# Kernel optimization log

Hardware: AMD Instinct MI355X
Metric: run time of the kernel (lower is better)

Reference implementation:

```python
import jax, jax.numpy as jnp
import numpy as np

N_NODES = 50000
N_EDGES = 1600000
IN_DIM = 128
OUT_DIM = 128


def setup_inputs() -> dict:
    key = jax.random.key(0)
    k_h, k_e, k_wm, k_wu, k_bu = jax.random.split(key, 5)
    h = jax.random.normal(k_h, (N_NODES, IN_DIM), dtype=jnp.float32)
    edge_index = jax.random.randint(k_e, (2, N_EDGES), 0, N_NODES, dtype=jnp.int64)
    # nn.Linear weights: W_msg [out, in] no bias; W_upd [out, in+out] with bias
    s1 = 1.0 / np.sqrt(IN_DIM)
    s2 = 1.0 / np.sqrt(IN_DIM + OUT_DIM)
    W_msg = jax.random.uniform(k_wm, (OUT_DIM, IN_DIM), jnp.float32, -s1, s1)
    W_upd = jax.random.uniform(k_wu, (OUT_DIM, IN_DIM + OUT_DIM), jnp.float32, -s2, s2)
    b_upd = jax.random.uniform(k_bu, (OUT_DIM,), jnp.float32, -s2, s2)
    return {"h": h, "edge_index": edge_index, "W_msg": W_msg, "W_upd": W_upd, "b_upd": b_upd}


def reference(h, edge_index, W_msg, W_upd, b_upd):
    src, dst = edge_index[0], edge_index[1]
    # gather -> linear: messages [E, out_dim]
    messages = jnp.einsum("ei,oi->eo", h[src], W_msg)
    # scatter-add aggregation into [N, out_dim]
    agg = jax.ops.segment_sum(messages, dst, num_segments=h.shape[0])
    # concat -> linear -> relu
    hu = jnp.concatenate([h, agg], axis=1)
    return jax.nn.relu(jnp.einsum("ni,oi->no", hu, W_upd) + b_upd)
```

## Files before the change

### kernel.cpp

```cpp
#include <hip/hip_runtime.h>
#include <hip/hip_bf16.h>

#define NN   50000
#define NE   1600000
#define D    128
#define NBUK 391
#define CAP  5120
#define EPB  4096
#define ASTR 136

typedef __attribute__((ext_vector_type(8))) short short8;
typedef __attribute__((ext_vector_type(4))) float f32x4;

__device__ __forceinline__ unsigned short f2b(float x) {
  unsigned u = __float_as_uint(x);
  u += 0x7fffu + ((u >> 16) & 1u);
  return (unsigned short)(u >> 16);
}
__device__ __forceinline__ float b2f(unsigned short v) {
  return __uint_as_float(((unsigned)v) << 16);
}

__global__ __launch_bounds__(256) void init_k(const float* __restrict__ h,
                                              unsigned short* __restrict__ hb,
                                              int* __restrict__ gcur,
                                              const float* __restrict__ Wm,
                                              const float* __restrict__ Wu,
                                              unsigned short* __restrict__ W1b,
                                              unsigned short* __restrict__ Wcb,
                                              const int* __restrict__ ei,
                                              int* __restrict__ flg) {
  __shared__ int nz;
  const int blk = blockIdx.x;
  if (blk < 6250) {
    int i = blk * 256 + threadIdx.x;
    float4 x = ((const float4*)h)[i];
    ushort4 o;
    o.x = f2b(x.x); o.y = f2b(x.y); o.z = f2b(x.z); o.w = f2b(x.w);
    ((ushort4*)hb)[i] = o;
    if (i < NBUK) gcur[i] = 0;
  } else if (blk < 6314) {
    int tid = (blk - 6250) * 256 + threadIdx.x;
    int o = tid >> 7, j = tid & 127;
    W1b[tid] = f2b(Wu[o * 256 + j]);
    float acc = 0.f;
#pragma unroll 4
    for (int k = 0; k < 128; ++k)
      acc += Wu[o * 256 + 128 + k] * Wm[k * 128 + j];
    Wcb[tid] = f2b(acc);
  } else {
    if (threadIdx.x == 0) nz = 0;
    __syncthreads();
    int idx = 1 + 2 * ((int)threadIdx.x * (NE / 256));
    if (ei[idx] != 0) atomicOr(&nz, 1);
    __syncthreads();
    if (threadIdx.x == 0) *flg = (nz == 0) ? 1 : 0;
  }
}

__global__ __launch_bounds__(512) void bfill_k(const int* __restrict__ ei,
                                               const int* __restrict__ flag,
                                               int* __restrict__ gcur,
                                               unsigned* __restrict__ ebuf) {
  __shared__ int cnt[NBUK];
  __shared__ int off[NBUK];
  const int tid = threadIdx.x;
  if (tid < NBUK) cnt[tid] = 0;
  __syncthreads();
  const int f = *flag;
  const int e0 = blockIdx.x * EPB + tid * 8;
  unsigned pk[8]; int bk[8]; int lr[8];
  if (e0 + 8 <= NE) {
    int sv[8], dv[8];
    if (f) {
      const int4* ps = (const int4*)(ei + 2 * (size_t)e0);
      const int4* pd = (const int4*)(ei + 2 * (size_t)NE + 2 * (size_t)e0);
      int4 a = ps[0], b = ps[1], c = ps[2], d = ps[3];
      sv[0]=a.x; sv[1]=a.z; sv[2]=b.x; sv[3]=b.z; sv[4]=c.x; sv[5]=c.z; sv[6]=d.x; sv[7]=d.z;
      a = pd[0]; b = pd[1]; c = pd[2]; d = pd[3];
      dv[0]=a.x; dv[1]=a.z; dv[2]=b.x; dv[3]=b.z; dv[4]=c.x; dv[5]=c.z; dv[6]=d.x; dv[7]=d.z;
    } else {
      const int4* ps = (const int4*)(ei + e0);
      const int4* pd = (const int4*)(ei + (size_t)NE + e0);
      int4 a = ps[0], b = ps[1];
      sv[0]=a.x; sv[1]=a.y; sv[2]=a.z; sv[3]=a.w; sv[4]=b.x; sv[5]=b.y; sv[6]=b.z; sv[7]=b.w;
      a = pd[0]; b = pd[1];
      dv[0]=a.x; dv[1]=a.y; dv[2]=a.z; dv[3]=a.w; dv[4]=b.x; dv[5]=b.y; dv[6]=b.z; dv[7]=b.w;
    }
#pragma unroll
    for (int j = 0; j < 8; ++j) {
      bk[j] = dv[j] >> 7;
      pk[j] = (unsigned)sv[j] | ((unsigned)(dv[j] & 127) << 16);
      lr[j] = atomicAdd(&cnt[bk[j]], 1);
    }
  } else {
    for (int j = 0; j < 8; ++j) {
      int e = e0 + j;
      bk[j] = -1;
      if (e < NE) {
        int src = f ? ei[2 * (size_t)e] : ei[e];
        int dst = f ? ei[2 * ((size_t)NE + e)] : ei[NE + e];
        bk[j] = dst >> 7;
        pk[j] = (unsigned)src | ((unsigned)(dst & 127) << 16);
        lr[j] = atomicAdd(&cnt[bk[j]], 1);
      }
    }
  }
  __syncthreads();
  if (tid < NBUK)
    off[tid] = cnt[tid] ? atomicAdd(&gcur[tid], cnt[tid]) : 0;
  __syncthreads();
#pragma unroll
  for (int j = 0; j < 8; ++j) {
    if (bk[j] >= 0) {
      int idx = off[bk[j]] + lr[j];
      if (idx < CAP) ebuf[(size_t)bk[j] * CAP + idx] = pk[j];
    }
  }
}

__global__ __launch_bounds__(1024, 8) void sortagg_k(const unsigned* __restrict__ ebuf,
                                                     const int* __restrict__ gcur,
                                                     const unsigned short* __restrict__ hb,
                                                     const unsigned short* __restrict__ W1b,
                                                     const unsigned short* __restrict__ Wcb,
                                                     const float* __restrict__ bias,
                                                     float* __restrict__ out) {
  __shared__ unsigned short srt[CAP];
  __shared__ __align__(16) unsigned short aggL[128 * ASTR];
  __shared__ int cnt[128];
  __shared__ int ofs[129];
  __shared__ int cur[128];
  __shared__ int wsum[2];
  const int b = blockIdx.x, tid = threadIdx.x;
  const int lane = tid & 63, wv = tid >> 6;
  if (tid < 128) cnt[tid] = 0;
  __syncthreads();
  const int count = min(gcur[b], CAP);
  const unsigned* eb = ebuf + (size_t)b * CAP;
  for (int e = tid; e < count; e += 1024)
    atomicAdd(&cnt[eb[e] >> 16], 1);
  __syncthreads();
  int v = 0, s = 0;
  if (tid < 128) {
    v = cnt[tid]; s = v;
#pragma unroll
    for (int d = 1; d < 64; d <<= 1) {
      int t = __shfl_up(s, d, 64);
      if (lane >= d) s += t;
    }
    if (lane == 63) wsum[wv] = s;
  }
  __syncthreads();
  if (tid < 128) {
    int excl = (wv ? wsum[0] : 0) + s - v;
    ofs[tid] = excl;
    cur[tid] = excl;
  }
  if (tid == 0) ofs[128] = count;
  __syncthreads();
  for (int e = tid; e < count; e += 1024) {
    unsigned p = eb[e];
    int slot = atomicAdd(&cur[p >> 16], 1);
    srt[slot] = (unsigned short)(p & 0xffffu);
  }
  __syncthreads();

  const int l2 = lane * 2;
  const unsigned short* hbl = hb + l2;
#pragma unroll 1
  for (int k = 0; k < 8; ++k) {
    const int n = wv * 8 + k;
    const int beg = ofs[n], end = ofs[n + 1];
    float ax0 = 0.f, ay0 = 0.f, ax1 = 0.f, ay1 = 0.f;
    int e = beg;
    for (; e + 16 <= end; e += 16) {
      unsigned vv[16];
#pragma unroll
      for (int j = 0; j < 16; ++j)
        vv[j] = *(const unsigned*)(hbl + (size_t)srt[e + j] * D);
#pragma unroll
      for (int j = 0; j < 16; j += 2) {
        ax0 += b2f((unsigned short)(vv[j] & 0xffffu));
        ay0 += b2f((unsigned short)(vv[j] >> 16));
        ax1 += b2f((unsigned short)(vv[j + 1] & 0xffffu));
        ay1 += b2f((unsigned short)(vv[j + 1] >> 16));
      }
    }
    for (; e + 4 <= end; e += 4) {
      unsigned vv[4];
#pragma unroll
      for (int j = 0; j < 4; ++j)
        vv[j] = *(const unsigned*)(hbl + (size_t)srt[e + j] * D);
#pragma unroll
      for (int j = 0; j < 4; j += 2) {
        ax0 += b2f((unsigned short)(vv[j] & 0xffffu));
        ay0 += b2f((unsigned short)(vv[j] >> 16));
        ax1 += b2f((unsigned short)(vv[j + 1] & 0xffffu));
        ay1 += b2f((unsigned short)(vv[j + 1] >> 16));
      }
    }
    for (; e < end; ++e) {
      unsigned vv = *(const unsigned*)(hbl + (size_t)srt[e] * D);
      ax0 += b2f((unsigned short)(vv & 0xffffu));
      ay0 += b2f((unsigned short)(vv >> 16));
    }
    unsigned o = (unsigned)f2b(ax0 + ax1) | ((unsigned)f2b(ay0 + ay1) << 16);
    ((unsigned*)aggL)[n * (ASTR / 2) + lane] = o;
  }
  __syncthreads();

  const int r = lane & 15, g = lane >> 4;
  const int tile = wv >> 1;
  const int t0 = (wv & 1) * 4;
  const int rowL = tile * 16 + r;
  const int nodeA = min(b * 128 + rowL, NN - 1);

  f32x4 acc[4];
#pragma unroll
  for (int t = 0; t < 4; ++t) acc[t] = (f32x4){0.f, 0.f, 0.f, 0.f};

#pragma unroll
  for (int c = 0; c < 8; ++c) {
    const int k0 = (c & 3) * 32 + g * 8;
    short8 a;
    if (c < 4) {
      a = *(const short8*)(hb + (size_t)nodeA * D + k0);
    } else {
      a = *(const short8*)(aggL + rowL * ASTR + k0);
    }
    const unsigned short* W = (c < 4) ? W1b : Wcb;
#pragma unroll
    for (int tt = 0; tt < 4; ++tt) {
      short8 bfr = *(const short8*)(W + (size_t)((t0 + tt) * 16 + r) * D + k0);
      acc[tt] = __builtin_amdgcn_mfma_f32_16x16x32_bf16(a, bfr, acc[tt], 0, 0, 0);
    }
  }

#pragma unroll
  for (int tt = 0; tt < 4; ++tt) {
    const int col = (t0 + tt) * 16 + r;
    const float bv = bias[col];
#pragma unroll
    for (int j = 0; j < 4; ++j) {
      const int orow = b * 128 + tile * 16 + g * 4 + j;
      if (orow < NN) {
        float vv = acc[tt][j] + bv;
        out[(size_t)orow * D + col] = vv > 0.f ? vv : 0.f;
      }
    }
  }
}

extern "C" void kernel_launch(void* const* d_in, const int* in_sizes, int n_in,
                              void* d_out, int out_size, void* d_ws, size_t ws_size,
                              hipStream_t stream) {
  const float* h  = (const float*)d_in[0];
  const int*   ei = (const int*)d_in[1];
  const float* Wm = (const float*)d_in[2];
  const float* Wu = (const float*)d_in[3];
  const float* bu = (const float*)d_in[4];
  float* out = (float*)d_out;

  char* ws = (char*)d_ws;
  unsigned short* hb   = (unsigned short*)(ws);
  unsigned*       ebuf = (unsigned*)(ws + 12800000);
  int*            gcur = (int*)(ws + 20807680);
  unsigned short* W1b  = (unsigned short*)(ws + 20809728);
  unsigned short* Wcb  = (unsigned short*)(ws + 20842496);
  int*            flg  = (int*)(ws + 20875264);

  init_k<<<6315, 256, 0, stream>>>(h, hb, gcur, Wm, Wu, W1b, Wcb, ei, flg);
  bfill_k<<<(NE + EPB - 1) / EPB, 512, 0, stream>>>(ei, flg, gcur, ebuf);
  sortagg_k<<<NBUK, 1024, 0, stream>>>(ebuf, gcur, hb, W1b, Wcb, bu, out);
}
```

Before: 117.4 us.

## Fuse prep and bucket-fill kernels, widen gather loads, halve aggregation block size

Merges the bf16 conversion, weight folding, index-format detection and edge bucketing into one launch, replacing the gcur reset with a memset and computing the int64 flag inside each bucketing block. The aggregation kernel now runs 512 threads. Each wave handles 16 nodes, with 16-byte gathers spread over four edges per lane group and a shuffle reduction at the end. Each wave then computes a full 16x128 MFMA output tile. This aims to cut launch overhead and raise memory-level parallelism in the gather, at the cost of more registers per thread and redundant flag reads in every bucketing block.

```diff
diff --git a/kernel.cpp b/kernel.cpp
--- a/kernel.cpp
+++ b/kernel.cpp
@@ -8,6 +8,8 @@
 #define CAP  5120
 #define EPB  4096
 #define ASTR 136
+#define PREP_BLKS 3125
+#define WPREP_BLKS 32
 
 typedef __attribute__((ext_vector_type(8))) short short8;
 typedef __attribute__((ext_vector_type(4))) float f32x4;
@@ -17,58 +19,60 @@
   u += 0x7fffu + ((u >> 16) & 1u);
   return (unsigned short)(u >> 16);
 }
-__device__ __forceinline__ float b2f(unsigned short v) {
-  return __uint_as_float(((unsigned)v) << 16);
-}
-
-__global__ __launch_bounds__(256) void init_k(const float* __restrict__ h,
-                                              unsigned short* __restrict__ hb,
-                                              int* __restrict__ gcur,
-                                              const float* __restrict__ Wm,
-                                              const float* __restrict__ Wu,
-                                              unsigned short* __restrict__ W1b,
-                                              unsigned short* __restrict__ Wcb,
-                                              const int* __restrict__ ei,
-                                              int* __restrict__ flg) {
-  __shared__ int nz;
-  const int blk = blockIdx.x;
-  if (blk < 6250) {
-    int i = blk * 256 + threadIdx.x;
-    float4 x = ((const float4*)h)[i];
-    ushort4 o;
-    o.x = f2b(x.x); o.y = f2b(x.y); o.z = f2b(x.z); o.w = f2b(x.w);
-    ((ushort4*)hb)[i] = o;
-    if (i < NBUK) gcur[i] = 0;
-  } else if (blk < 6314) {
-    int tid = (blk - 6250) * 256 + threadIdx.x;
-    int o = tid >> 7, j = tid & 127;
-    W1b[tid] = f2b(Wu[o * 256 + j]);
-    float acc = 0.f;
-#pragma unroll 4
-    for (int k = 0; k < 128; ++k)
-      acc += Wu[o * 256 + 128 + k] * Wm[k * 128 + j];
-    Wcb[tid] = f2b(acc);
-  } else {
-    if (threadIdx.x == 0) nz = 0;
-    __syncthreads();
-    int idx = 1 + 2 * ((int)threadIdx.x * (NE / 256));
-    if (ei[idx] != 0) atomicOr(&nz, 1);
-    __syncthreads();
-    if (threadIdx.x == 0) *flg = (nz == 0) ? 1 : 0;
-  }
-}
-
-__global__ __launch_bounds__(512) void bfill_k(const int* __restrict__ ei,
-                                               const int* __restrict__ flag,
+__device__ __forceinline__ float b2f(unsigned v) {
+  return __uint_as_float(v << 16);
+}
+__device__ __forceinline__ float b2fh(unsigned v) {
+  return __uint_as_float(v & 0xffff0000u);
+}
+
+__global__ __launch_bounds__(512) void fused_k(const float* __restrict__ h,
+                                               unsigned short* __restrict__ hb,
                                                int* __restrict__ gcur,
+                                               const float* __restrict__ Wm,
+                                               const float* __restrict__ Wu,
+                                               unsigned short* __restrict__ W1b,
+                                               unsigned short* __restrict__ Wcb,
+                                               const int* __restrict__ ei,
                                                unsigned* __restrict__ ebuf) {
   __shared__ int cnt[NBUK];
   __shared__ int off[NBUK];
-  const int tid = threadIdx.x;
+  __shared__ int nz;
+  const int blk = blockIdx.x, tid = threadIdx.x;
+
+  if (blk >= NBUK) {
+    if (blk < NBUK + PREP_BLKS) {
+      int i = (blk - NBUK) * 512 + tid;
+      float4 x = ((const float4*)h)[i];
+      ushort4 o;
+      o.x = f2b(x.x); o.y = f2b(x.y); o.z = f2b(x.z); o.w = f2b(x.w);
+      ((ushort4*)hb)[i] = o;
+    } else {
+      int t2 = (blk - NBUK - PREP_BLKS) * 512 + tid;
+      if (t2 < 16384) {
+        int o = t2 >> 7, j = t2 & 127;
+        W1b[t2] = f2b(Wu[o * 256 + j]);
+        float acc = 0.f;
+#pragma unroll 4
+        for (int k = 0; k < 128; ++k)
+          acc += Wu[o * 256 + 128 + k] * Wm[k * 128 + j];
+        Wcb[t2] = f2b(acc);
+      }
+    }
+    return;
+  }
+
+  if (tid == 0) nz = 0;
   if (tid < NBUK) cnt[tid] = 0;
   __syncthreads();
-  const int f = *flag;
-  const int e0 = blockIdx.x * EPB + tid * 8;
+  if (tid < 256) {
+    int idx = 1 + 2 * (tid * (NE / 256));
+    if (ei[idx] != 0) atomicOr(&nz, 1);
+  }
+  __syncthreads();
+  const int f = (nz == 0);
+
+  const int e0 = blk * EPB + tid * 8;
   unsigned pk[8]; int bk[8]; int lr[8];
   if (e0 + 8 <= NE) {
     int sv[8], dv[8];
@@ -119,13 +123,13 @@
   }
 }
 
-__global__ __launch_bounds__(1024, 8) void sortagg_k(const unsigned* __restrict__ ebuf,
-                                                     const int* __restrict__ gcur,
-                                                     const unsigned short* __restrict__ hb,
-                                                     const unsigned short* __restrict__ W1b,
-                                                     const unsigned short* __restrict__ Wcb,
-                                                     const float* __restrict__ bias,
-                                                     float* __restrict__ out) {
+__global__ __launch_bounds__(512, 6) void sortagg_k(const unsigned* __restrict__ ebuf,
+                                                    const int* __restrict__ gcur,
+                                                    const unsigned short* __restrict__ hb,
+                                                    const unsigned short* __restrict__ W1b,
+                                                    const unsigned short* __restrict__ Wcb,
+                                                    const float* __restrict__ bias,
+                                                    float* __restrict__ out) {
   __shared__ unsigned short srt[CAP];
   __shared__ __align__(16) unsigned short aggL[128 * ASTR];
   __shared__ int cnt[128];
@@ -138,7 +142,7 @@
   __syncthreads();
   const int count = min(gcur[b], CAP);
   const unsigned* eb = ebuf + (size_t)b * CAP;
-  for (int e = tid; e < count; e += 1024)
+  for (int e = tid; e < count; e += 512)
     atomicAdd(&cnt[eb[e] >> 16], 1);
   __syncthreads();
   int v = 0, s = 0;
@@ -159,66 +163,71 @@
   }
   if (tid == 0) ofs[128] = count;
   __syncthreads();
-  for (int e = tid; e < count; e += 1024) {
+  for (int e = tid; e < count; e += 512) {
     unsigned p = eb[e];
     int slot = atomicAdd(&cur[p >> 16], 1);
     srt[slot] = (unsigned short)(p & 0xffffu);
   }
   __syncthreads();
 
-  const int l2 = lane * 2;
-  const unsigned short* hbl = hb + l2;
+  const int q = lane >> 4;
+  const int r = lane & 15;
+  const unsigned short* hbl = hb + r * 8;
 #pragma unroll 1
-  for (int k = 0; k < 8; ++k) {
-    const int n = wv * 8 + k;
+  for (int k = 0; k < 16; ++k) {
+    const int n = wv * 16 + k;
     const int beg = ofs[n], end = ofs[n + 1];
-    float ax0 = 0.f, ay0 = 0.f, ax1 = 0.f, ay1 = 0.f;
+    float a0=0.f,a1=0.f,a2=0.f,a3=0.f,a4=0.f,a5=0.f,a6=0.f,a7=0.f;
     int e = beg;
-    for (; e + 16 <= end; e += 16) {
-      unsigned vv[16];
-#pragma unroll
-      for (int j = 0; j < 16; ++j)
-        vv[j] = *(const unsigned*)(hbl + (size_t)srt[e + j] * D);
-#pragma unroll
-      for (int j = 0; j < 16; j += 2) {
-        ax0 += b2f((unsigned short)(vv[j] & 0xffffu));
-        ay0 += b2f((unsigned short)(vv[j] >> 16));
-        ax1 += b2f((unsigned short)(vv[j + 1] & 0xffffu));
-        ay1 += b2f((unsigned short)(vv[j + 1] >> 16));
-      }
-    }
-    for (; e + 4 <= end; e += 4) {
-      unsigned vv[4];
-#pragma unroll
-      for (int j = 0; j < 4; ++j)
-        vv[j] = *(const unsigned*)(hbl + (size_t)srt[e + j] * D);
-#pragma unroll
-      for (int j = 0; j < 4; j += 2) {
-        ax0 += b2f((unsigned short)(vv[j] & 0xffffu));
-        ay0 += b2f((unsigned short)(vv[j] >> 16));
-        ax1 += b2f((unsigned short)(vv[j + 1] & 0xffffu));
-        ay1 += b2f((unsigned short)(vv[j + 1] >> 16));
-      }
-    }
-    for (; e < end; ++e) {
-      unsigned vv = *(const unsigned*)(hbl + (size_t)srt[e] * D);
-      ax0 += b2f((unsigned short)(vv & 0xffffu));
-      ay0 += b2f((unsigned short)(vv >> 16));
-    }
-    unsigned o = (unsigned)f2b(ax0 + ax1) | ((unsigned)f2b(ay0 + ay1) << 16);
-    ((unsigned*)aggL)[n * (ASTR / 2) + lane] = o;
-  }
-  __syncthreads();
-
-  const int r = lane & 15, g = lane >> 4;
-  const int tile = wv >> 1;
-  const int t0 = (wv & 1) * 4;
-  const int rowL = tile * 16 + r;
+    for (; e + 32 <= end; e += 32) {
+      uint4 vv[8];
+#pragma unroll
+      for (int j = 0; j < 8; ++j)
+        vv[j] = *(const uint4*)(hbl + (size_t)srt[e + 4 * j + q] * D);
+#pragma unroll
+      for (int j = 0; j < 8; ++j) {
+        a0 += b2f(vv[j].x & 0xffffu); a1 += b2fh(vv[j].x);
+        a2 += b2f(vv[j].y & 0xffffu); a3 += b2fh(vv[j].y);
+        a4 += b2f(vv[j].z & 0xffffu); a5 += b2fh(vv[j].z);
+        a6 += b2f(vv[j].w & 0xffffu); a7 += b2fh(vv[j].w);
+      }
+    }
+    for (; e < end; e += 4) {
+      int edge = e + q;
+      int ce = min(edge, end - 1);
+      uint4 vv = *(const uint4*)(hbl + (size_t)srt[ce] * D);
+      if (edge >= end) { vv.x = 0u; vv.y = 0u; vv.z = 0u; vv.w = 0u; }
+      a0 += b2f(vv.x & 0xffffu); a1 += b2fh(vv.x);
+      a2 += b2f(vv.y & 0xffffu); a3 += b2fh(vv.y);
+      a4 += b2f(vv.z & 0xffffu); a5 += b2fh(vv.z);
+      a6 += b2f(vv.w & 0xffffu); a7 += b2fh(vv.w);
+    }
+    a0 += __shfl_xor(a0, 16, 64); a0 += __shfl_xor(a0, 32, 64);
+    a1 += __shfl_xor(a1, 16, 64); a1 += __shfl_xor(a1, 32, 64);
+    a2 += __shfl_xor(a2, 16, 64); a2 += __shfl_xor(a2, 32, 64);
+    a3 += __shfl_xor(a3, 16, 64); a3 += __shfl_xor(a3, 32, 64);
+    a4 += __shfl_xor(a4, 16, 64); a4 += __shfl_xor(a4, 32, 64);
+    a5 += __shfl_xor(a5, 16, 64); a5 += __shfl_xor(a5, 32, 64);
+    a6 += __shfl_xor(a6, 16, 64); a6 += __shfl_xor(a6, 32, 64);
+    a7 += __shfl_xor(a7, 16, 64); a7 += __shfl_xor(a7, 32, 64);
+    if (lane < 16) {
+      uint4 o;
+      o.x = (unsigned)f2b(a0) | ((unsigned)f2b(a1) << 16);
+      o.y = (unsigned)f2b(a2) | ((unsigned)f2b(a3) << 16);
+      o.z = (unsigned)f2b(a4) | ((unsigned)f2b(a5) << 16);
+      o.w = (unsigned)f2b(a6) | ((unsigned)f2b(a7) << 16);
+      *(uint4*)(aggL + n * ASTR + r * 8) = o;
+    }
+  }
+  __syncthreads();
+
+  const int rr = lane & 15, g = lane >> 4;
+  const int rowL = wv * 16 + rr;
   const int nodeA = min(b * 128 + rowL, NN - 1);
 
-  f32x4 acc[4];
-#pragma unroll
-  for (int t = 0; t < 4; ++t) acc[t] = (f32x4){0.f, 0.f, 0.f, 0.f};
+  f32x4 acc[8];
+#pragma unroll
+  for (int t = 0; t < 8; ++t) acc[t] = (f32x4){0.f, 0.f, 0.f, 0.f};
 
 #pragma unroll
   for (int c = 0; c < 8; ++c) {
@@ -231,21 +240,21 @@
     }
     const unsigned short* W = (c < 4) ? W1b : Wcb;
 #pragma unroll
-    for (int tt = 0; tt < 4; ++tt) {
-      short8 bfr = *(const short8*)(W + (size_t)((t0 + tt) * 16 + r) * D + k0);
-      acc[tt] = __builtin_amdgcn_mfma_f32_16x16x32_bf16(a, bfr, acc[tt], 0, 0, 0);
-    }
-  }
-
-#pragma unroll
-  for (int tt = 0; tt < 4; ++tt) {
-    const int col = (t0 + tt) * 16 + r;
+    for (int t = 0; t < 8; ++t) {
+      short8 bfr = *(const short8*)(W + (size_t)(t * 16 + rr) * D + k0);
+      acc[t] = __builtin_amdgcn_mfma_f32_16x16x32_bf16(a, bfr, acc[t], 0, 0, 0);
+    }
+  }
+
+#pragma unroll
+  for (int t = 0; t < 8; ++t) {
+    const int col = t * 16 + rr;
     const float bv = bias[col];
 #pragma unroll
     for (int j = 0; j < 4; ++j) {
-      const int orow = b * 128 + tile * 16 + g * 4 + j;
+      const int orow = b * 128 + wv * 16 + g * 4 + j;
       if (orow < NN) {
-        float vv = acc[tt][j] + bv;
+        float vv = acc[t][j] + bv;
         out[(size_t)orow * D + col] = vv > 0.f ? vv : 0.f;
       }
     }
@@ -268,9 +277,9 @@
   int*            gcur = (int*)(ws + 20807680);
   unsigned short* W1b  = (unsigned short*)(ws + 20809728);
   unsigned short* Wcb  = (unsigned short*)(ws + 20842496);
-  int*            flg  = (int*)(ws + 20875264);
-
-  init_k<<<6315, 256, 0, stream>>>(h, hb, gcur, Wm, Wu, W1b, Wcb, ei, flg);
-  bfill_k<<<(NE + EPB - 1) / EPB, 512, 0, stream>>>(ei, flg, gcur, ebuf);
-  sortagg_k<<<NBUK, 1024, 0, stream>>>(ebuf, gcur, hb, W1b, Wcb, bu, out);
-}
+
+  hipMemsetAsync(gcur, 0, NBUK * sizeof(int), stream);
+  fused_k<<<NBUK + PREP_BLKS + WPREP_BLKS, 512, 0, stream>>>(
+      h, hb, gcur, Wm, Wu, W1b, Wcb, ei, ebuf);
+  sortagg_k<<<NBUK, 512, 0, stream>>>(ebuf, gcur, hb, W1b, Wcb, bu, out);
+}
```

Result: slower. 126.4 us (+7.6%).
